# Kernel tuning notes

Measured on AMD Instinct MI355X. Metric: run time of the kernel, lower is better.

## Reference

```python
import jax, jax.numpy as jnp
import numpy as np

# Surrogate spike: heaviside forward, straight-through (identity) gradient,
# consistent with the repo's Dampener (identity fwd, 1.0*grad bwd) convention.
@jax.custom_vjp
def spike(x):
    return (x > 0).astype(x.dtype)

def _spike_fwd(x):
    return spike(x), None

def _spike_bwd(_, g):
    return (g,)

spike.defvjp(_spike_fwd, _spike_bwd)

T, B = 1024, 64
NI, NPRE, NAD, NPOST, NOUT = 512, 2048, 1024, 2048, 512
FF_LEAK = 0.5  # feedback coefficient of the ff_spk cell (assumed LIF-style)


def setup_inputs() -> dict:
    key = jax.random.key(0)
    ks = jax.random.split(key, 9)

    def lin(kw, kb, out_f, in_f):
        s = 1.0 / np.sqrt(in_f)
        W = jax.random.uniform(kw, (out_f, in_f), jnp.float32, -s, s)
        b = jax.random.uniform(kb, (out_f,), jnp.float32, -s, s)
        return W, b

    W_pre, b_pre = lin(ks[0], ks[1], NPRE, NI + NAD)
    W_ad, b_ad = lin(ks[2], ks[3], NAD, NPRE)
    W_post, b_post = lin(ks[4], ks[5], NPOST, NI + NAD)
    W_out, b_out = lin(ks[6], ks[7], NOUT, NPOST)
    inp = jax.random.normal(ks[8], (T, B, NI), jnp.float32)
    return {"inp": inp, "W_pre": W_pre, "b_pre": b_pre, "W_ad": W_ad,
            "b_ad": b_ad, "W_post": W_post, "b_post": b_post,
            "W_out": W_out, "b_out": b_out}


def reference(inp, W_pre, b_pre, W_ad, b_ad, W_post, b_post, W_out, b_out):
    bsz = inp.shape[1]
    nad = W_ad.shape[0]
    hz = nad // 2
    # h = None path: half zeros, half ones
    spikes0 = jnp.concatenate(
        [jnp.zeros((bsz, hz), inp.dtype), jnp.ones((bsz, nad - hz), inp.dtype)], axis=1)

    def step(spikes, inp_t):
        # Dampener is identity in forward (grad scale 1.0) -> no-op
        x = jnp.concatenate([inp_t, spikes], axis=1)        # [B, NI+NAD]
        pre = spike(x @ W_pre.T + b_pre)                    # [B, NPRE]
        ad = pre @ W_ad.T + b_ad                            # [B, NAD]
        # ff_spk: LIF-style cell with spike feedback; returns (out, new_state)
        new_spikes = spike(ad + FF_LEAK * spikes)           # [B, NAD]
        y = jnp.concatenate([inp_t, new_spikes], axis=1)    # [B, NI+NAD]
        post = spike(y @ W_post.T + b_post)                 # [B, NPOST]
        o = post @ W_out.T + b_out                          # [B, NOUT]
        return new_spikes, o

    final_spikes, output = jax.lax.scan(step, spikes0, inp)
    return output, final_spikes
```

## Files before the change

### kernel.cpp

```cpp
#include <hip/hip_runtime.h>
#include <stdint.h>


#define TT 1024
#define BB 64
#define NIc 512
#define NPREc 2048
#define NADc 1024
#define NPOSTc 2048
#define NOUTc 512
#define KXc 1536

typedef unsigned long long u64;

__global__ __launch_bounds__(256) void k_init(u64* __restrict__ spk_bits,
                                              uint8_t* __restrict__ spk_u8) {
  int tid = blockIdx.x * 256 + threadIdx.x;
  int b = tid >> 10, i = tid & 1023;
  spk_u8[b * NADc + i] = (uint8_t)((i < 512) ? 0 : 1);
  if (tid < NADc) spk_bits[tid] = (tid < 512) ? 0ull : ~0ull;
}

__global__ __launch_bounds__(256) void k_stage1(
    const float* __restrict__ inp, const float* __restrict__ W_pre,
    const float* __restrict__ b_pre, const uint8_t* __restrict__ spk_u8,
    uint8_t* __restrict__ pre_u8, int t) {
  const int lane = threadIdx.x & 63;
  const int wave = threadIdx.x >> 6;
  int j0 = (blockIdx.x * 4 + wave) * 2;
  j0 = __builtin_amdgcn_readfirstlane(j0);
  const int b = lane;
  const float* xrow = inp + ((size_t)t * BB + b) * NIc;
  const float* w0 = W_pre + (size_t)j0 * KXc;
  const float* w1 = w0 + KXc;
  const uint8_t* srow = spk_u8 + b * NADc;
  float a0 = 0.f, a1 = 0.f;
  for (int i = 0; i < NIc; i += 4) {
    float4 x = *(const float4*)(xrow + i);
    float4 p = *(const float4*)(w0 + i);
    float4 q = *(const float4*)(w1 + i);
    a0 = fmaf(x.x, p.x, a0); a0 = fmaf(x.y, p.y, a0);
    a0 = fmaf(x.z, p.z, a0); a0 = fmaf(x.w, p.w, a0);
    a1 = fmaf(x.x, q.x, a1); a1 = fmaf(x.y, q.y, a1);
    a1 = fmaf(x.z, q.z, a1); a1 = fmaf(x.w, q.w, a1);
  }
  for (int k = 0; k < NADc; k += 4) {
    uchar4 xc = *(const uchar4*)(srow + k);
    float x0 = (float)xc.x, x1 = (float)xc.y, x2 = (float)xc.z, x3 = (float)xc.w;
    float4 p = *(const float4*)(w0 + NIc + k);
    float4 q = *(const float4*)(w1 + NIc + k);
    a0 = fmaf(x0, p.x, a0); a0 = fmaf(x1, p.y, a0);
    a0 = fmaf(x2, p.z, a0); a0 = fmaf(x3, p.w, a0);
    a1 = fmaf(x0, q.x, a1); a1 = fmaf(x1, q.y, a1);
    a1 = fmaf(x2, q.z, a1); a1 = fmaf(x3, q.w, a1);
  }
  float s0 = a0 + b_pre[j0];
  float s1 = a1 + b_pre[j0 + 1];
  uint16_t pk = (uint16_t)((s0 > 0.f) ? 1u : 0u) |
                (uint16_t)(((s1 > 0.f) ? 1u : 0u) << 8);
  *(uint16_t*)(pre_u8 + b * NPREc + j0) = pk;
}

__global__ __launch_bounds__(256) void k_stage2(
    const float* __restrict__ W_ad, const float* __restrict__ b_ad,
    const uint8_t* __restrict__ pre_u8, const u64* __restrict__ spk_bits_old,
    u64* __restrict__ spk_bits_next, uint8_t* __restrict__ spk_u8) {
  const int lane = threadIdx.x & 63;
  const int wave = threadIdx.x >> 6;
  int i = blockIdx.x * 4 + wave;
  i = __builtin_amdgcn_readfirstlane(i);
  const int b = lane;
  const float* wrow = W_ad + (size_t)i * NPREc;
  const uint8_t* prow = pre_u8 + b * NPREc;
  float a = 0.f;
  for (int j = 0; j < NPREc; j += 4) {
    uchar4 xc = *(const uchar4*)(prow + j);
    float4 w = *(const float4*)(wrow + j);
    a = fmaf((float)xc.x, w.x, a); a = fmaf((float)xc.y, w.y, a);
    a = fmaf((float)xc.z, w.z, a); a = fmaf((float)xc.w, w.w, a);
  }
  float ad = a + b_ad[i];
  u64 ow = spk_bits_old[i];
  float os = (float)((unsigned)(ow >> b) & 1u);
  float v = ad + 0.5f * os;
  int nb = (v > 0.f) ? 1 : 0;
  u64 mask = __ballot(nb);
  if (lane == 0) spk_bits_next[i] = mask;
  spk_u8[b * NADc + i] = (uint8_t)nb;
}

__global__ __launch_bounds__(256) void k_post(
    const float* __restrict__ inp, const float* __restrict__ W_post,
    const float* __restrict__ b_post, const u64* __restrict__ spk_bits,
    u64* __restrict__ post_bits) {
  const int t = blockIdx.x;
  const int lane = threadIdx.x & 63;
  const int wave = threadIdx.x >> 6;
  int j0 = (blockIdx.y * 4 + wave) * 16;
  j0 = __builtin_amdgcn_readfirstlane(j0);
  const int b = lane;
  const float* xrow = inp + ((size_t)t * BB + b) * NIc;
  const u64* sbits = spk_bits + (size_t)(t + 1) * NADc;
  const float* wbase = W_post + (size_t)j0 * KXc;
  float acc[16];
#pragma unroll
  for (int q = 0; q < 16; ++q) acc[q] = 0.f;
  for (int i = 0; i < NIc; i += 4) {
    float4 x = *(const float4*)(xrow + i);
#pragma unroll
    for (int q = 0; q < 16; ++q) {
      float4 w = *(const float4*)(wbase + (size_t)q * KXc + i);
      acc[q] = fmaf(x.x, w.x, acc[q]); acc[q] = fmaf(x.y, w.y, acc[q]);
      acc[q] = fmaf(x.z, w.z, acc[q]); acc[q] = fmaf(x.w, w.w, acc[q]);
    }
  }
  for (int k = 0; k < NADc; k += 4) {
    float xs0 = (float)((unsigned)(sbits[k + 0] >> b) & 1u);
    float xs1 = (float)((unsigned)(sbits[k + 1] >> b) & 1u);
    float xs2 = (float)((unsigned)(sbits[k + 2] >> b) & 1u);
    float xs3 = (float)((unsigned)(sbits[k + 3] >> b) & 1u);
#pragma unroll
    for (int q = 0; q < 16; ++q) {
      float4 w = *(const float4*)(wbase + (size_t)q * KXc + NIc + k);
      acc[q] = fmaf(xs0, w.x, acc[q]); acc[q] = fmaf(xs1, w.y, acc[q]);
      acc[q] = fmaf(xs2, w.z, acc[q]); acc[q] = fmaf(xs3, w.w, acc[q]);
    }
  }
#pragma unroll
  for (int q = 0; q < 16; ++q) {
    float s = acc[q] + b_post[j0 + q];
    u64 m = __ballot(s > 0.f);
    if (lane == 0) post_bits[(size_t)t * NPOSTc + j0 + q] = m;
  }
}

__global__ __launch_bounds__(256) void k_out(
    const float* __restrict__ W_out, const float* __restrict__ b_out,
    const u64* __restrict__ post_bits, float* __restrict__ out) {
  const int t = blockIdx.x;
  const int lane = threadIdx.x & 63;
  const int wave = threadIdx.x >> 6;
  int n0 = (blockIdx.y * 4 + wave) * 16;
  n0 = __builtin_amdgcn_readfirstlane(n0);
  const int b = lane;
  const u64* pb = post_bits + (size_t)t * NPOSTc;
  const float* wbase = W_out + (size_t)n0 * NPOSTc;
  float acc[16];
#pragma unroll
  for (int q = 0; q < 16; ++q) acc[q] = 0.f;
  for (int j = 0; j < NPOSTc; j += 4) {
    float xs0 = (float)((unsigned)(pb[j + 0] >> b) & 1u);
    float xs1 = (float)((unsigned)(pb[j + 1] >> b) & 1u);
    float xs2 = (float)((unsigned)(pb[j + 2] >> b) & 1u);
    float xs3 = (float)((unsigned)(pb[j + 3] >> b) & 1u);
#pragma unroll
    for (int q = 0; q < 16; ++q) {
      float4 w = *(const float4*)(wbase + (size_t)q * NPOSTc + j);
      acc[q] = fmaf(xs0, w.x, acc[q]); acc[q] = fmaf(xs1, w.y, acc[q]);
      acc[q] = fmaf(xs2, w.z, acc[q]); acc[q] = fmaf(xs3, w.w, acc[q]);
    }
  }
  float* orow = out + ((size_t)t * BB + b) * NOUTc;
#pragma unroll
  for (int q = 0; q < 16; ++q) orow[n0 + q] = acc[q] + b_out[n0 + q];
}

__global__ __launch_bounds__(256) void k_final(const u64* __restrict__ spk_last,
                                               float* __restrict__ out_tail) {
  int tid = blockIdx.x * 256 + threadIdx.x;
  int b = tid >> 10, i = tid & 1023;
  out_tail[tid] = (float)((unsigned)(spk_last[i] >> b) & 1u);
}

extern "C" void kernel_launch(void* const* d_in, const int* in_sizes, int n_in,
                              void* d_out, int out_size, void* d_ws, size_t ws_size,
                              hipStream_t stream) {
  const float* inp    = (const float*)d_in[0];
  const float* W_pre  = (const float*)d_in[1];
  const float* b_pre  = (const float*)d_in[2];
  const float* W_ad   = (const float*)d_in[3];
  const float* b_ad   = (const float*)d_in[4];
  const float* W_post = (const float*)d_in[5];
  const float* b_post = (const float*)d_in[6];
  const float* W_out  = (const float*)d_in[7];
  const float* b_out  = (const float*)d_in[8];
  float* out = (float*)d_out;

  char* ws = (char*)d_ws;
  u64* spk_bits  = (u64*)ws;
  u64* post_bits = (u64*)(ws + 8396800);
  uint8_t* spk_u8 = (uint8_t*)(ws + 8396800 + 16777216);
  uint8_t* pre_u8 = spk_u8 + 65536;

  k_init<<<256, 256, 0, stream>>>(spk_bits, spk_u8);

  for (int t = 0; t < TT; ++t) {
    k_stage1<<<256, 256, 0, stream>>>(inp, W_pre, b_pre, spk_u8, pre_u8, t);
    k_stage2<<<256, 256, 0, stream>>>(W_ad, b_ad, pre_u8,
                                      spk_bits + (size_t)t * NADc,
                                      spk_bits + (size_t)(t + 1) * NADc,
                                      spk_u8);
  }

  k_post<<<dim3(TT, 32), 256, 0, stream>>>(inp, W_post, b_post, spk_bits, post_bits);
  k_out<<<dim3(TT, 8), 256, 0, stream>>>(W_out, b_out, post_bits, out);
  k_final<<<256, 256, 0, stream>>>(spk_bits + (size_t)TT * NADc,
                                   out + (size_t)TT * BB * NOUTc);
}
```

Measured before the change: 70.54 ms.

## Fuse recurrent loop into one persistent kernel with software grid barriers

Replaces the 2048 per-timestep kernel launches of the sequential recurrence with a single persistent kernel of 256 blocks. The blocks synchronise through an atomic-counter grid barrier and keep activations in float buffers in a k-interleaved layout, so each lane does coalesced float4 loads. It also prefetches the next step's input during stage 2. This is meant to remove launch overhead and inter-kernel gaps, but it depends on all 256 blocks being co-resident and adds barrier spin cost.

New measurement: 185.9 ms. 164% more time.

```diff
diff --git a/kernel.cpp b/kernel.cpp
--- a/kernel.cpp
+++ b/kernel.cpp
@@ -10,83 +10,129 @@
 #define NPOSTc 2048
 #define NOUTc 512
 #define KXc 1536
+#define NBLK 256
 
 typedef unsigned long long u64;
 
-__global__ __launch_bounds__(256) void k_init(u64* __restrict__ spk_bits,
-                                              uint8_t* __restrict__ spk_u8) {
-  int tid = blockIdx.x * 256 + threadIdx.x;
-  int b = tid >> 10, i = tid & 1023;
-  spk_u8[b * NADc + i] = (uint8_t)((i < 512) ? 0 : 1);
-  if (tid < NADc) spk_bits[tid] = (tid < 512) ? 0ull : ~0ull;
-}
-
-__global__ __launch_bounds__(256) void k_stage1(
+__global__ void k_bar_init(unsigned* __restrict__ bar) {
+  if (threadIdx.x < 64) bar[threadIdx.x] = 0u;
+}
+
+__device__ __forceinline__ void gbar(unsigned* cnt, unsigned* gen, unsigned target) {
+  __syncthreads();
+  if (threadIdx.x == 0) {
+    __threadfence();
+    unsigned prev = __hip_atomic_fetch_add(cnt, 1u, __ATOMIC_ACQ_REL,
+                                           __HIP_MEMORY_SCOPE_AGENT);
+    if (prev == (unsigned)NBLK * target - 1u) {
+      __hip_atomic_store(gen, target, __ATOMIC_RELEASE, __HIP_MEMORY_SCOPE_AGENT);
+    } else {
+      while (__hip_atomic_load(gen, __ATOMIC_ACQUIRE, __HIP_MEMORY_SCOPE_AGENT) < target)
+        __builtin_amdgcn_s_sleep(1);
+    }
+    __threadfence();
+  }
+  __syncthreads();
+}
+
+__global__ __launch_bounds__(256, 4) void rbnn_seq(
     const float* __restrict__ inp, const float* __restrict__ W_pre,
-    const float* __restrict__ b_pre, const uint8_t* __restrict__ spk_u8,
-    uint8_t* __restrict__ pre_u8, int t) {
+    const float* __restrict__ b_pre, const float* __restrict__ W_ad,
+    const float* __restrict__ b_ad, float* __restrict__ preP,
+    float* __restrict__ actA, float* __restrict__ actB,
+    u64* __restrict__ spk_bits, unsigned* __restrict__ bar) {
+  unsigned* cnt = bar;
+  unsigned* gen = bar + 32;
   const int lane = threadIdx.x & 63;
-  const int wave = threadIdx.x >> 6;
-  int j0 = (blockIdx.x * 4 + wave) * 2;
-  j0 = __builtin_amdgcn_readfirstlane(j0);
-  const int b = lane;
-  const float* xrow = inp + ((size_t)t * BB + b) * NIc;
-  const float* w0 = W_pre + (size_t)j0 * KXc;
-  const float* w1 = w0 + KXc;
-  const uint8_t* srow = spk_u8 + b * NADc;
-  float a0 = 0.f, a1 = 0.f;
-  for (int i = 0; i < NIc; i += 4) {
-    float4 x = *(const float4*)(xrow + i);
-    float4 p = *(const float4*)(w0 + i);
-    float4 q = *(const float4*)(w1 + i);
-    a0 = fmaf(x.x, p.x, a0); a0 = fmaf(x.y, p.y, a0);
-    a0 = fmaf(x.z, p.z, a0); a0 = fmaf(x.w, p.w, a0);
-    a1 = fmaf(x.x, q.x, a1); a1 = fmaf(x.y, q.y, a1);
-    a1 = fmaf(x.z, q.z, a1); a1 = fmaf(x.w, q.w, a1);
-  }
-  for (int k = 0; k < NADc; k += 4) {
-    uchar4 xc = *(const uchar4*)(srow + k);
-    float x0 = (float)xc.x, x1 = (float)xc.y, x2 = (float)xc.z, x3 = (float)xc.w;
-    float4 p = *(const float4*)(w0 + NIc + k);
-    float4 q = *(const float4*)(w1 + NIc + k);
-    a0 = fmaf(x0, p.x, a0); a0 = fmaf(x1, p.y, a0);
-    a0 = fmaf(x2, p.z, a0); a0 = fmaf(x3, p.w, a0);
-    a1 = fmaf(x0, q.x, a1); a1 = fmaf(x1, q.y, a1);
-    a1 = fmaf(x2, q.z, a1); a1 = fmaf(x3, q.w, a1);
-  }
-  float s0 = a0 + b_pre[j0];
-  float s1 = a1 + b_pre[j0 + 1];
-  uint16_t pk = (uint16_t)((s0 > 0.f) ? 1u : 0u) |
-                (uint16_t)(((s1 > 0.f) ? 1u : 0u) << 8);
-  *(uint16_t*)(pre_u8 + b * NPREc + j0) = pk;
-}
-
-__global__ __launch_bounds__(256) void k_stage2(
-    const float* __restrict__ W_ad, const float* __restrict__ b_ad,
-    const uint8_t* __restrict__ pre_u8, const u64* __restrict__ spk_bits_old,
-    u64* __restrict__ spk_bits_next, uint8_t* __restrict__ spk_u8) {
-  const int lane = threadIdx.x & 63;
-  const int wave = threadIdx.x >> 6;
-  int i = blockIdx.x * 4 + wave;
-  i = __builtin_amdgcn_readfirstlane(i);
-  const int b = lane;
-  const float* wrow = W_ad + (size_t)i * NPREc;
-  const uint8_t* prow = pre_u8 + b * NPREc;
-  float a = 0.f;
-  for (int j = 0; j < NPREc; j += 4) {
-    uchar4 xc = *(const uchar4*)(prow + j);
-    float4 w = *(const float4*)(wrow + j);
-    a = fmaf((float)xc.x, w.x, a); a = fmaf((float)xc.y, w.y, a);
-    a = fmaf((float)xc.z, w.z, a); a = fmaf((float)xc.w, w.w, a);
-  }
-  float ad = a + b_ad[i];
-  u64 ow = spk_bits_old[i];
-  float os = (float)((unsigned)(ow >> b) & 1u);
-  float v = ad + 0.5f * os;
-  int nb = (v > 0.f) ? 1 : 0;
-  u64 mask = __ballot(nb);
-  if (lane == 0) spk_bits_next[i] = mask;
-  spk_u8[b * NADc + i] = (uint8_t)nb;
+  const int w = __builtin_amdgcn_readfirstlane((int)(threadIdx.x >> 6));
+  const int blk = blockIdx.x;
+  unsigned tgt = 1;
+
+  if (w == 0) {
+    int r0 = blk * 2;
+    float2 v;
+    v.x = inp[(size_t)lane * NIc + r0];
+    v.y = inp[(size_t)lane * NIc + r0 + 1];
+    *(float2*)(actA + (r0 >> 2) * 256 + lane * 4 + (r0 & 3)) = v;
+  } else if (w == 1) {
+    float one = (blk >= 128) ? 1.f : 0.f;
+    float4 v; v.x = one; v.y = one; v.z = one; v.w = one;
+    *(float4*)(actA + (128 + blk) * 256 + lane * 4) = v;
+    if (lane < 4) spk_bits[blk * 4 + lane] = (blk >= 128) ? ~0ull : 0ull;
+  }
+  gbar(cnt, gen, tgt); ++tgt;
+
+  for (int t = 0; t < TT; ++t) {
+    const float* cur = (t & 1) ? actB : actA;
+    float* nxt = (t & 1) ? actA : actB;
+
+    {
+      const int j0 = blk * 8 + w * 2;
+      const float* wp0 = W_pre + (size_t)j0 * KXc;
+      const float* wp1 = wp0 + KXc;
+      const float* ap = cur + lane * 4;
+      float a0 = 0.f, a1 = 0.f;
+#pragma unroll 4
+      for (int kk = 0; kk < 384; ++kk) {
+        float4 x = *(const float4*)(ap + kk * 256);
+        float4 p = *(const float4*)(wp0 + kk * 4);
+        float4 q = *(const float4*)(wp1 + kk * 4);
+        a0 = fmaf(x.x, p.x, a0); a0 = fmaf(x.y, p.y, a0);
+        a0 = fmaf(x.z, p.z, a0); a0 = fmaf(x.w, p.w, a0);
+        a1 = fmaf(x.x, q.x, a1); a1 = fmaf(x.y, q.y, a1);
+        a1 = fmaf(x.z, q.z, a1); a1 = fmaf(x.w, q.w, a1);
+      }
+      float s0 = a0 + b_pre[j0];
+      float s1 = a1 + b_pre[j0 + 1];
+      float2 pv;
+      pv.x = (s0 > 0.f) ? 1.f : 0.f;
+      pv.y = (s1 > 0.f) ? 1.f : 0.f;
+      *(float2*)(preP + (j0 >> 2) * 256 + lane * 4 + (j0 & 3)) = pv;
+    }
+    gbar(cnt, gen, tgt); ++tgt;
+
+    if (w < 2) {
+      const int i0 = blk * 4 + w * 2;
+      const float* wa0 = W_ad + (size_t)i0 * NPREc;
+      const float* wa1 = wa0 + NPREc;
+      const float* pp = preP + lane * 4;
+      float a0 = 0.f, a1 = 0.f;
+#pragma unroll 4
+      for (int jj = 0; jj < 512; ++jj) {
+        float4 x = *(const float4*)(pp + jj * 256);
+        float4 p = *(const float4*)(wa0 + jj * 4);
+        float4 q = *(const float4*)(wa1 + jj * 4);
+        a0 = fmaf(x.x, p.x, a0); a0 = fmaf(x.y, p.y, a0);
+        a0 = fmaf(x.z, p.z, a0); a0 = fmaf(x.w, p.w, a0);
+        a1 = fmaf(x.x, q.x, a1); a1 = fmaf(x.y, q.y, a1);
+        a1 = fmaf(x.z, q.z, a1); a1 = fmaf(x.w, q.w, a1);
+      }
+      const int r0 = 512 + i0;
+      const int pbase = (r0 >> 2) * 256 + lane * 4 + (r0 & 3);
+      float os0 = cur[pbase];
+      float os1 = cur[pbase + 1];
+      float ad0 = a0 + b_ad[i0];
+      float ad1 = a1 + b_ad[i0 + 1];
+      float v0 = ad0 + 0.5f * os0;
+      float v1 = ad1 + 0.5f * os1;
+      int nb0 = (v0 > 0.f) ? 1 : 0;
+      int nb1 = (v1 > 0.f) ? 1 : 0;
+      float2 nv; nv.x = (float)nb0; nv.y = (float)nb1;
+      *(float2*)(nxt + pbase) = nv;
+      u64 m0 = __ballot(nb0);
+      u64 m1 = __ballot(nb1);
+      if (lane == 0) {
+        spk_bits[(size_t)(t + 1) * NADc + i0] = m0;
+        spk_bits[(size_t)(t + 1) * NADc + i0 + 1] = m1;
+      }
+    } else if (w == 2 && t + 1 < TT) {
+      int r0 = blk * 2;
+      const float* xr = inp + ((size_t)(t + 1) * BB + lane) * NIc;
+      float2 v; v.x = xr[r0]; v.y = xr[r0 + 1];
+      *(float2*)(nxt + (r0 >> 2) * 256 + lane * 4 + (r0 & 3)) = v;
+    }
+    gbar(cnt, gen, tgt); ++tgt;
+  }
 }
 
 __global__ __launch_bounds__(256) void k_post(
@@ -189,19 +235,14 @@
   char* ws = (char*)d_ws;
   u64* spk_bits  = (u64*)ws;
   u64* post_bits = (u64*)(ws + 8396800);
-  uint8_t* spk_u8 = (uint8_t*)(ws + 8396800 + 16777216);
-  uint8_t* pre_u8 = spk_u8 + 65536;
-
-  k_init<<<256, 256, 0, stream>>>(spk_bits, spk_u8);
-
-  for (int t = 0; t < TT; ++t) {
-    k_stage1<<<256, 256, 0, stream>>>(inp, W_pre, b_pre, spk_u8, pre_u8, t);
-    k_stage2<<<256, 256, 0, stream>>>(W_ad, b_ad, pre_u8,
-                                      spk_bits + (size_t)t * NADc,
-                                      spk_bits + (size_t)(t + 1) * NADc,
-                                      spk_u8);
-  }
-
+  float* preP    = (float*)(ws + 25174016);
+  float* actA    = (float*)(ws + 25698304);
+  float* actB    = (float*)(ws + 26091520);
+  unsigned* bar  = (unsigned*)(ws + 26484736);
+
+  k_bar_init<<<1, 64, 0, stream>>>(bar);
+  rbnn_seq<<<NBLK, 256, 0, stream>>>(inp, W_pre, b_pre, W_ad, b_ad,
+                                     preP, actA, actB, spk_bits, bar);
   k_post<<<dim3(TT, 32), 256, 0, stream>>>(inp, W_post, b_post, spk_bits, post_bits);
   k_out<<<dim3(TT, 8), 256, 0, stream>>>(W_out, b_out, post_bits, out);
   k_final<<<256, 256, 0, stream>>>(spk_bits + (size_t)TT * NADc,
```
